# Kernel tuning notes

Measured on AMD Instinct MI355X. Metric: run time of the kernel, lower is better.

The kernel has to match this reference:

```python
import jax, jax.numpy as jnp
import numpy as np

B, S, D, H, O, E, K = 4, 2048, 1024, 2048, 1024, 8, 2

def setup_inputs() -> dict:
    key = jax.random.key(0)
    ks = jax.random.split(key, 8)
    x = jax.random.normal(ks[0], (B, S, D), dtype=jnp.float32)
    # kaiming-uniform-ish scale for weights, zero biases (as in _init_w)
    gate_w = jax.random.uniform(ks[1], (E, D), dtype=jnp.float32, minval=-1, maxval=1) * np.sqrt(6.0 / D)
    gate_b = jnp.zeros((E,), dtype=jnp.float32)
    w1 = jax.random.uniform(ks[2], (E, D, H), dtype=jnp.float32, minval=-1, maxval=1) * np.sqrt(6.0 / D)
    b1 = jnp.zeros((E, H), dtype=jnp.float32)
    w2 = jax.random.uniform(ks[3], (E, H, O), dtype=jnp.float32, minval=-1, maxval=1) * np.sqrt(6.0 / H)
    b2 = jnp.zeros((E, O), dtype=jnp.float32)
    return {"x": x, "gate_w": gate_w, "gate_b": gate_b, "w1": w1, "b1": b1, "w2": w2, "b2": b2}

def reference(x, gate_w, gate_b, w1, b1, w2, b2):
    # gate: softmax over experts, then top-k (k=2)
    logits = jnp.einsum('bsd,ed->bse', x, gate_w) + gate_b          # [B,S,E]
    probs = jax.nn.softmax(logits, axis=-1)
    topk_vals, topk_idx = jax.lax.top_k(probs, K)                    # [B,S,K]
    # dense all-expert MLPs (Linear-ReLU-Linear), dropout = 0
    h = jax.nn.relu(jnp.einsum('bsd,edh->bseh', x, w1) + b1)         # [B,S,E,H]
    expert_out = jnp.einsum('bseh,eho->bseo', h, w2) + b2            # [B,S,E,O]
    # gather top-k experts and combine with gate weights
    sel = jnp.take_along_axis(expert_out, topk_idx[..., None], axis=2)  # [B,S,K,O]
    return jnp.sum(sel * topk_vals[..., None], axis=2)               # [B,S,O]
```

## Files before the change

kernel.cpp:

```cpp
#include <hip/hip_runtime.h>

#define T_TOKENS 8192
#define D_DIM 1024
#define H_DIM 2048
#define O_DIM 1024
#define E_NUM 8
#define NPAIR 16384
#define GY_MAX 136

typedef unsigned short u16;
typedef __bf16 bf16x8 __attribute__((ext_vector_type(8)));
typedef float f32x4 __attribute__((ext_vector_type(4)));

__device__ inline u16 f2bf(float f) {
  union { float f; unsigned u; } v; v.f = f;
  unsigned r = v.u + 0x7FFFu + ((v.u >> 16) & 1u);
  return (u16)(r >> 16);
}

__device__ __forceinline__ void gload16(const u16* g, u16* l) {
  __builtin_amdgcn_global_load_lds((const __attribute__((address_space(1))) void*)g,
                                   (__attribute__((address_space(3))) void*)l, 16, 0, 0);
}

__global__ void transpose_cvt_kernel(const float* __restrict__ w, u16* __restrict__ wt,
                                     int R, int C) {
  __shared__ float tile[32][33];
  int e = blockIdx.z;
  int c0 = blockIdx.x * 32, r0 = blockIdx.y * 32;
  const float* wp = w + (size_t)e * R * C;
  u16* wtp = wt + (size_t)e * R * C;
  int tx = threadIdx.x, ty = threadIdx.y;
  #pragma unroll
  for (int j = 0; j < 32; j += 8)
    tile[ty + j][tx] = wp[(size_t)(r0 + ty + j) * C + c0 + tx];
  __syncthreads();
  #pragma unroll
  for (int j = 0; j < 32; j += 8)
    wtp[(size_t)(c0 + ty + j) * R + r0 + tx] = f2bf(tile[tx][ty + j]);
}

__global__ void gate_kernel(const float* __restrict__ x, const float* __restrict__ gw,
                            const float* __restrict__ gb, int* __restrict__ topk_idx,
                            float* __restrict__ topk_val, u16* __restrict__ xb) {
  int t = blockIdx.x * 4 + (threadIdx.x >> 6);
  int lane = threadIdx.x & 63;
  const float4* xr4 = (const float4*)(x + (size_t)t * D_DIM);
  const float4* gw4 = (const float4*)gw;
  u16* xbr = xb + (size_t)t * D_DIM;
  float acc[E_NUM];
  #pragma unroll
  for (int e = 0; e < E_NUM; e++) acc[e] = 0.f;
  #pragma unroll
  for (int it = 0; it < D_DIM / 256; ++it) {
    float4 xv = xr4[it * 64 + lane];
    ushort4 o;
    o.x = f2bf(xv.x); o.y = f2bf(xv.y); o.z = f2bf(xv.z); o.w = f2bf(xv.w);
    *(ushort4*)(xbr + (it * 64 + lane) * 4) = o;
    #pragma unroll
    for (int e = 0; e < E_NUM; e++) {
      float4 wv = gw4[e * (D_DIM / 4) + it * 64 + lane];
      acc[e] += xv.x * wv.x + xv.y * wv.y + xv.z * wv.z + xv.w * wv.w;
    }
  }
  #pragma unroll
  for (int e = 0; e < E_NUM; e++) {
    #pragma unroll
    for (int o = 32; o > 0; o >>= 1) acc[e] += __shfl_down(acc[e], o);
  }
  if (lane == 0) {
    float l[E_NUM], mx = -1e30f;
    #pragma unroll
    for (int e = 0; e < E_NUM; e++) { l[e] = acc[e] + gb[e]; mx = fmaxf(mx, l[e]); }
    float p[E_NUM], s = 0.f;
    #pragma unroll
    for (int e = 0; e < E_NUM; e++) { p[e] = expf(l[e] - mx); s += p[e]; }
    float inv = 1.f / s;
    int i1 = 0;
    #pragma unroll
    for (int e = 1; e < E_NUM; e++) if (p[e] > p[i1]) i1 = e;
    int i2 = (i1 == 0) ? 1 : 0;
    #pragma unroll
    for (int e = 0; e < E_NUM; e++) if (e != i1 && e != i2 && p[e] > p[i2]) i2 = e;
    topk_idx[t * 2] = i1;     topk_idx[t * 2 + 1] = i2;
    topk_val[t * 2] = p[i1] * inv; topk_val[t * 2 + 1] = p[i2] * inv;
  }
}

__global__ void histscan_kernel(const int* __restrict__ topk_idx,
                                int* __restrict__ counts, int* __restrict__ eoff,
                                int* __restrict__ nblk, int* __restrict__ tbl_e,
                                int* __restrict__ tbl_m0) {
  __shared__ int wh[4][E_NUM];
  int tid = threadIdx.x;
  int lane = tid & 63, wave = tid >> 6;
  int myc = 0;
  for (int i = tid; i < NPAIR; i += 256) {
    int e = topk_idx[i];
    #pragma unroll
    for (int ee = 0; ee < E_NUM; ee++) {
      unsigned long long m = __ballot(e == ee);
      if (lane == ee) myc += __popcll(m);
    }
  }
  if (lane < E_NUM) wh[wave][lane] = myc;
  __syncthreads();
  if (tid == 0) {
    int s = 0, cl[E_NUM];
    for (int e = 0; e < E_NUM; e++) {
      int c = wh[0][e] + wh[1][e] + wh[2][e] + wh[3][e];
      counts[e] = c;
      cl[e] = c;
      eoff[e] = s;
      s += c;
    }
    eoff[E_NUM] = s;
    int nb = 0;
    for (int e = 0; e < E_NUM; e++)
      for (int m0 = 0; m0 < cl[e]; m0 += 128) { tbl_e[nb] = e; tbl_m0[nb] = m0; nb++; }
    nblk[0] = nb;
  }
}

__global__ void scatter_kernel(const int* __restrict__ topk_idx, const float* __restrict__ topk_val,
                               const int* __restrict__ eoff, int* __restrict__ cursor_pad,
                               int* __restrict__ pair_token, float* __restrict__ pair_gate) {
  __shared__ int lhist[E_NUM];
  __shared__ int lbase[E_NUM];
  int tid = threadIdx.x;
  int t = blockIdx.x * 256 + tid;
  if (tid < E_NUM) lhist[tid] = 0;
  __syncthreads();
  int e0 = topk_idx[t * 2], e1 = topk_idx[t * 2 + 1];
  int r0 = atomicAdd(&lhist[e0], 1);
  int r1 = atomicAdd(&lhist[e1], 1);
  __syncthreads();
  if (tid < E_NUM) lbase[tid] = eoff[tid] + atomicAdd(&cursor_pad[tid * 32], lhist[tid]);
  __syncthreads();
  int p0 = lbase[e0] + r0;
  int p1 = lbase[e1] + r1;
  pair_token[p0] = t; pair_gate[p0] = topk_val[t * 2];
  pair_token[p1] = t; pair_gate[p1] = topk_val[t * 2 + 1];
}


__global__ __launch_bounds__(256, 2) void gemm1_kernel(
    const u16* __restrict__ xb, const u16* __restrict__ w1t, const float* __restrict__ b1,
    const int* __restrict__ pair_token, const int* __restrict__ eoff,
    const int* __restrict__ ecnt, const int* __restrict__ nblk,
    const int* __restrict__ tbl_e, const int* __restrict__ tbl_m0,
    u16* __restrict__ hbuf) {
  int lin = blockIdx.y * 16 + blockIdx.x;
  int swz = (lin & 7) * (16 * GY_MAX / 8) + (lin >> 3);
  const int bx = swz & 15;
  const int yb = swz >> 4;
  if (yb >= nblk[0]) return;
  const int e = tbl_e[yb];
  const int m0t = tbl_m0[yb];
  const int ne = ecnt[e];
  const int off = eoff[e];
  const int n0 = bx * 128;

  __shared__ __align__(16) u16 As0[128 * 64], As1[128 * 64];
  __shared__ __align__(16) u16 Bs0[128 * 64], Bs1[128 * 64];

  const int tid = threadIdx.x;
  const int wid = tid >> 6;
  const int lane = tid & 63;

  const int strow8 = lane >> 3;
  const int slot = lane & 7;
  const u16* aptr[4]; const u16* bptr[4];
  #pragma unroll
  for (int j = 0; j < 4; j++) {
    int r = wid * 32 + j * 8 + strow8;
    int gm = m0t + r;
    int tok = (gm < ne) ? pair_token[off + gm] : 0;
    int gl = slot ^ (r & 7);
    aptr[j] = xb + (size_t)tok * D_DIM + gl * 8;
    bptr[j] = w1t + ((size_t)e * H_DIM + (n0 + r)) * D_DIM + gl * 8;
  }

  const int wm = (wid & 1) * 64;
  const int wn = (wid >> 1) * 64;
  const int lrow = lane & 15;
  const int quad = lane >> 4;
  const int pg0 = quad ^ (lrow & 7);
  const int pg1 = (quad + 4) ^ (lrow & 7);

  f32x4 acc[4][4] = {};

  auto STAGE = [&](u16* A_, u16* B_, int kk) {
    #pragma unroll
    for (int j = 0; j < 4; j++) {
      gload16(aptr[j] + kk, A_ + wid * 2048 + j * 512);
      gload16(bptr[j] + kk, B_ + wid * 2048 + j * 512);
    }
  };
  auto COMPUTE = [&](const u16* A_, const u16* B_) {
    bf16x8 af[4], bfr[4];
    #pragma unroll
    for (int i = 0; i < 4; i++) af[i] = *(const bf16x8*)&A_[(wm + i * 16 + lrow) * 64 + pg0 * 8];
    #pragma unroll
    for (int j = 0; j < 4; j++) bfr[j] = *(const bf16x8*)&B_[(wn + j * 16 + lrow) * 64 + pg0 * 8];
    #pragma unroll
    for (int i = 0; i < 4; i++)
      #pragma unroll
      for (int j = 0; j < 4; j++)
        acc[i][j] = __builtin_amdgcn_mfma_f32_16x16x32_bf16(af[i], bfr[j], acc[i][j], 0, 0, 0);
    #pragma unroll
    for (int i = 0; i < 4; i++) af[i] = *(const bf16x8*)&A_[(wm + i * 16 + lrow) * 64 + pg1 * 8];
    #pragma unroll
    for (int j = 0; j < 4; j++) bfr[j] = *(const bf16x8*)&B_[(wn + j * 16 + lrow) * 64 + pg1 * 8];
    #pragma unroll
    for (int i = 0; i < 4; i++)
      #pragma unroll
      for (int j = 0; j < 4; j++)
        acc[i][j] = __builtin_amdgcn_mfma_f32_16x16x32_bf16(af[i], bfr[j], acc[i][j], 0, 0, 0);
  };

  STAGE(As0, Bs0, 0);
  __syncthreads();
  for (int k0 = 0; k0 < D_DIM; k0 += 128) {
    if (k0 + 64 < D_DIM) STAGE(As1, Bs1, k0 + 64);
    COMPUTE(As0, Bs0);
    __syncthreads();
    if (k0 + 128 < D_DIM) STAGE(As0, Bs0, k0 + 128);
    COMPUTE(As1, Bs1);
    __syncthreads();
  }

  #pragma unroll
  for (int i = 0; i < 4; i++) {
    #pragma unroll
    for (int r = 0; r < 4; r++) {
      int m = wm + i * 16 + quad * 4 + r;
      int gm = m0t + m;
      if (gm >= ne) continue;
      size_t rowbase = (size_t)(off + gm) * H_DIM;
      #pragma unroll
      for (int j = 0; j < 4; j++) {
        int n = n0 + wn + j * 16 + lrow;
        float v = acc[i][j][r] + b1[e * H_DIM + n];
        v = v > 0.f ? v : 0.f;
        hbuf[rowbase + n] = f2bf(v);
      }
    }
  }
}

__global__ __launch_bounds__(256, 2) void gemm2_kernel(
    const u16* __restrict__ hbuf, const u16* __restrict__ w2t, const float* __restrict__ b2,
    const int* __restrict__ pair_token, const float* __restrict__ pair_gate,
    const int* __restrict__ eoff, const int* __restrict__ ecnt,
    const int* __restrict__ nblk, const int* __restrict__ tbl_e,
    const int* __restrict__ tbl_m0, float* __restrict__ out) {
  int lin = blockIdx.y * 8 + blockIdx.x;
  int swz = (lin & 7) * (8 * GY_MAX / 8) + (lin >> 3);
  const int bx = swz & 7;
  const int yb = swz >> 3;
  if (yb >= nblk[0]) return;
  const int e = tbl_e[yb];
  const int m0t = tbl_m0[yb];
  const int ne = ecnt[e];
  const int off = eoff[e];
  const int n0 = bx * 128;

  __shared__ __align__(16) u16 As0[128 * 64], As1[128 * 64];
  __shared__ __align__(16) u16 Bs0[128 * 64], Bs1[128 * 64];

  const int tid = threadIdx.x;
  const int wid = tid >> 6;
  const int lane = tid & 63;

  const int strow8 = lane >> 3;
  const int slot = lane & 7;
  const u16* aptr[4]; const u16* bptr[4];
  #pragma unroll
  for (int j = 0; j < 4; j++) {
    int r = wid * 32 + j * 8 + strow8;
    int gl = slot ^ (r & 7);
    aptr[j] = hbuf + (size_t)(off + m0t + r) * H_DIM + gl * 8;
    bptr[j] = w2t + ((size_t)e * O_DIM + (n0 + r)) * H_DIM + gl * 8;
  }

  const int wm = (wid & 1) * 64;
  const int wn = (wid >> 1) * 64;
  const int lrow = lane & 15;
  const int quad = lane >> 4;
  const int pg0 = quad ^ (lrow & 7);
  const int pg1 = (quad + 4) ^ (lrow & 7);

  f32x4 acc[4][4] = {};

  auto STAGE = [&](u16* A_, u16* B_, int kk) {
    #pragma unroll
    for (int j = 0; j < 4; j++) {
      gload16(aptr[j] + kk, A_ + wid * 2048 + j * 512);
      gload16(bptr[j] + kk, B_ + wid * 2048 + j * 512);
    }
  };
  auto COMPUTE = [&](const u16* A_, const u16* B_) {
    bf16x8 af[4], bfr[4];
    #pragma unroll
    for (int i = 0; i < 4; i++) af[i] = *(const bf16x8*)&A_[(wm + i * 16 + lrow) * 64 + pg0 * 8];
    #pragma unroll
    for (int j = 0; j < 4; j++) bfr[j] = *(const bf16x8*)&B_[(wn + j * 16 + lrow) * 64 + pg0 * 8];
    #pragma unroll
    for (int i = 0; i < 4; i++)
      #pragma unroll
      for (int j = 0; j < 4; j++)
        acc[i][j] = __builtin_amdgcn_mfma_f32_16x16x32_bf16(af[i], bfr[j], acc[i][j], 0, 0, 0);
    #pragma unroll
    for (int i = 0; i < 4; i++) af[i] = *(const bf16x8*)&A_[(wm + i * 16 + lrow) * 64 + pg1 * 8];
    #pragma unroll
    for (int j = 0; j < 4; j++) bfr[j] = *(const bf16x8*)&B_[(wn + j * 16 + lrow) * 64 + pg1 * 8];
    #pragma unroll
    for (int i = 0; i < 4; i++)
      #pragma unroll
      for (int j = 0; j < 4; j++)
        acc[i][j] = __builtin_amdgcn_mfma_f32_16x16x32_bf16(af[i], bfr[j], acc[i][j], 0, 0, 0);
  };

  STAGE(As0, Bs0, 0);
  __syncthreads();
  for (int k0 = 0; k0 < H_DIM; k0 += 128) {
    if (k0 + 64 < H_DIM) STAGE(As1, Bs1, k0 + 64);
    COMPUTE(As0, Bs0);
    __syncthreads();
    if (k0 + 128 < H_DIM) STAGE(As0, Bs0, k0 + 128);
    COMPUTE(As1, Bs1);
    __syncthreads();
  }

  #pragma unroll
  for (int i = 0; i < 4; i++) {
    #pragma unroll
    for (int r = 0; r < 4; r++) {
      int m = wm + i * 16 + quad * 4 + r;
      int gm = m0t + m;
      if (gm >= ne) continue;
      int pair = off + gm;
      int tok = pair_token[pair];
      float g = pair_gate[pair];
      #pragma unroll
      for (int j = 0; j < 4; j++) {
        int n = n0 + wn + j * 16 + lrow;
        float v = (acc[i][j][r] + b2[e * O_DIM + n]) * g;
        atomicAdd(&out[(size_t)tok * O_DIM + n], v);
      }
    }
  }
}

extern "C" void kernel_launch(void* const* d_in, const int* in_sizes, int n_in,
                              void* d_out, int out_size, void* d_ws, size_t ws_size,
                              hipStream_t stream) {
  const float* x  = (const float*)d_in[0];
  const float* gw = (const float*)d_in[1];
  const float* gb = (const float*)d_in[2];
  const float* w1 = (const float*)d_in[3];
  const float* b1 = (const float*)d_in[4];
  const float* w2 = (const float*)d_in[5];
  const float* b2 = (const float*)d_in[6];
  float* out = (float*)d_out;

  char* ws = (char*)d_ws;
  size_t off = 0;
  auto take = [&](size_t bytes) -> char* {
    char* p = ws + off;
    off = (off + bytes + 255) & ~(size_t)255;
    return p;
  };
  int*   meta       = (int*)take(4096);
  int*   cursor_pad = meta;
  int*   counts     = meta + 256;
  int*   eoff       = meta + 264;
  int*   nblk       = meta + 273;
  int*   tbl_e      = meta + 274;
  int*   tbl_m0     = meta + 410;
  int*   topk_idx   = (int*)take((size_t)T_TOKENS * 2 * 4);
  float* topk_val   = (float*)take((size_t)T_TOKENS * 2 * 4);
  int*   pair_token = (int*)take((size_t)(NPAIR + 256) * 4);
  float* pair_gate  = (float*)take((size_t)(NPAIR + 256) * 4);
  u16*   xb         = (u16*)take((size_t)T_TOKENS * D_DIM * 2);
  u16*   w1t        = (u16*)take((size_t)E_NUM * D_DIM * H_DIM * 2);
  u16*   w2t        = (u16*)take((size_t)E_NUM * H_DIM * O_DIM * 2);
  u16*   hbuf       = (u16*)take((size_t)(NPAIR + 128) * H_DIM * 2);

  hipMemsetAsync(meta, 0, 4096, stream);
  hipMemsetAsync(out, 0, (size_t)T_TOKENS * O_DIM * 4, stream);

  transpose_cvt_kernel<<<dim3(H_DIM / 32, D_DIM / 32, E_NUM), dim3(32, 8), 0, stream>>>(w1, w1t, D_DIM, H_DIM);
  transpose_cvt_kernel<<<dim3(O_DIM / 32, H_DIM / 32, E_NUM), dim3(32, 8), 0, stream>>>(w2, w2t, H_DIM, O_DIM);
  gate_kernel<<<T_TOKENS / 4, 256, 0, stream>>>(x, gw, gb, topk_idx, topk_val, xb);
  histscan_kernel<<<1, 256, 0, stream>>>(topk_idx, counts, eoff, nblk, tbl_e, tbl_m0);
  scatter_kernel<<<T_TOKENS / 256, 256, 0, stream>>>(topk_idx, topk_val, eoff, cursor_pad, pair_token, pair_gate);
  gemm1_kernel<<<dim3(16, GY_MAX), 256, 0, stream>>>(xb, w1t, b1, pair_token, eoff, counts, nblk, tbl_e, tbl_m0, hbuf);
  gemm2_kernel<<<dim3(8, GY_MAX), 256, 0, stream>>>(hbuf, w2t, b2, pair_token, pair_gate, eoff, counts, nblk, tbl_e, tbl_m0, out);
}
```

Measured before the change: 523.7 us.

## Use triple-buffered K=32 LDS pipeline with vmcnt waits in expert GEMMs

Both expert GEMM kernels move from a double-buffered K=64 stage to a three-stage ring of K=32 tiles (48KB LDS total), with a new packed two-rows-per-64-element swizzled layout. Each iteration waits with explicit s_waitcnt vmcnt instead of a full drain, so two future tiles stay in flight while the current one is computed. Launch bounds rise to 3 blocks per CU to raise occupancy. The cost is twice as many barriers per K, half as many MFMAs between barriers, and reliance on hand-counted vmcnt values, which is fragile if the compiler adds or reorders memory ops.

New measurement: 498.8 us. 1.05x faster.

```diff
diff --git a/kernel.cpp b/kernel.cpp
--- a/kernel.cpp
+++ b/kernel.cpp
@@ -11,6 +11,14 @@
 typedef unsigned short u16;
 typedef __bf16 bf16x8 __attribute__((ext_vector_type(8)));
 typedef float f32x4 __attribute__((ext_vector_type(4)));
+
+#define VMCNT(n) asm volatile("s_waitcnt vmcnt(" #n ")" ::: "memory")
+
+__device__ __forceinline__ void barsync() {
+  asm volatile("" ::: "memory");
+  __builtin_amdgcn_s_barrier();
+  __builtin_amdgcn_sched_barrier(0);
+}
 
 __device__ inline u16 f2bf(float f) {
   union { float f; unsigned u; } v; v.f = f;
@@ -144,7 +152,7 @@
 }
 
 
-__global__ __launch_bounds__(256, 2) void gemm1_kernel(
+__global__ __launch_bounds__(256, 3) void gemm1_kernel(
     const u16* __restrict__ xb, const u16* __restrict__ w1t, const float* __restrict__ b1,
     const int* __restrict__ pair_token, const int* __restrict__ eoff,
     const int* __restrict__ ecnt, const int* __restrict__ nblk,
@@ -161,57 +169,59 @@
   const int off = eoff[e];
   const int n0 = bx * 128;
 
-  __shared__ __align__(16) u16 As0[128 * 64], As1[128 * 64];
-  __shared__ __align__(16) u16 Bs0[128 * 64], Bs1[128 * 64];
+  __shared__ __align__(16) u16 SH[3 * 2 * 4096];
 
   const int tid = threadIdx.x;
   const int wid = tid >> 6;
   const int lane = tid & 63;
 
-  const int strow8 = lane >> 3;
-  const int slot = lane & 7;
-  const u16* aptr[4]; const u16* bptr[4];
-  #pragma unroll
-  for (int j = 0; j < 4; j++) {
-    int r = wid * 32 + j * 8 + strow8;
+  const u16* aptrA[2]; const u16* bptrB[2];
+  #pragma unroll
+  for (int j = 0; j < 2; j++) {
+    int p = wid * 16 + j * 8 + (lane >> 3);
+    int u = (lane & 7) ^ (p & 7);
+    int r = 2 * p + (u >> 2);
+    int c = u & 3;
     int gm = m0t + r;
     int tok = (gm < ne) ? pair_token[off + gm] : 0;
-    int gl = slot ^ (r & 7);
-    aptr[j] = xb + (size_t)tok * D_DIM + gl * 8;
-    bptr[j] = w1t + ((size_t)e * H_DIM + (n0 + r)) * D_DIM + gl * 8;
+    aptrA[j] = xb + (size_t)tok * D_DIM + c * 8;
+    bptrB[j] = w1t + ((size_t)e * H_DIM + (n0 + r)) * D_DIM + c * 8;
   }
 
   const int wm = (wid & 1) * 64;
   const int wn = (wid >> 1) * 64;
   const int lrow = lane & 15;
   const int quad = lane >> 4;
-  const int pg0 = quad ^ (lrow & 7);
-  const int pg1 = (quad + 4) ^ (lrow & 7);
 
   f32x4 acc[4][4] = {};
 
-  auto STAGE = [&](u16* A_, u16* B_, int kk) {
+  auto STAGE = [&](int buf, int k0) {
+    u16* Ab = SH + buf * 8192;
+    u16* Bb = Ab + 4096;
+    #pragma unroll
+    for (int j = 0; j < 2; j++) {
+      gload16(aptrA[j] + k0, Ab + (wid * 16 + j * 8) * 64);
+      gload16(bptrB[j] + k0, Bb + (wid * 16 + j * 8) * 64);
+    }
+  };
+  auto COMPUTE = [&](int buf) {
+    const u16* Ab = SH + buf * 8192;
+    const u16* Bb = Ab + 4096;
+    bf16x8 af[4], bfr[4];
+    #pragma unroll
+    for (int i = 0; i < 4; i++) {
+      int r = wm + i * 16 + lrow;
+      int p = r >> 1;
+      int s = (((r & 1) << 2) | quad) ^ (p & 7);
+      af[i] = *(const bf16x8*)&Ab[p * 64 + s * 8];
+    }
     #pragma unroll
     for (int j = 0; j < 4; j++) {
-      gload16(aptr[j] + kk, A_ + wid * 2048 + j * 512);
-      gload16(bptr[j] + kk, B_ + wid * 2048 + j * 512);
-    }
-  };
-  auto COMPUTE = [&](const u16* A_, const u16* B_) {
-    bf16x8 af[4], bfr[4];
-    #pragma unroll
-    for (int i = 0; i < 4; i++) af[i] = *(const bf16x8*)&A_[(wm + i * 16 + lrow) * 64 + pg0 * 8];
-    #pragma unroll
-    for (int j = 0; j < 4; j++) bfr[j] = *(const bf16x8*)&B_[(wn + j * 16 + lrow) * 64 + pg0 * 8];
-    #pragma unroll
-    for (int i = 0; i < 4; i++)
-      #pragma unroll
-      for (int j = 0; j < 4; j++)
-        acc[i][j] = __builtin_amdgcn_mfma_f32_16x16x32_bf16(af[i], bfr[j], acc[i][j], 0, 0, 0);
-    #pragma unroll
-    for (int i = 0; i < 4; i++) af[i] = *(const bf16x8*)&A_[(wm + i * 16 + lrow) * 64 + pg1 * 8];
-    #pragma unroll
-    for (int j = 0; j < 4; j++) bfr[j] = *(const bf16x8*)&B_[(wn + j * 16 + lrow) * 64 + pg1 * 8];
+      int r = wn + j * 16 + lrow;
+      int p = r >> 1;
+      int s = (((r & 1) << 2) | quad) ^ (p & 7);
+      bfr[j] = *(const bf16x8*)&Bb[p * 64 + s * 8];
+    }
     #pragma unroll
     for (int i = 0; i < 4; i++)
       #pragma unroll
@@ -219,16 +229,19 @@
         acc[i][j] = __builtin_amdgcn_mfma_f32_16x16x32_bf16(af[i], bfr[j], acc[i][j], 0, 0, 0);
   };
 
-  STAGE(As0, Bs0, 0);
-  __syncthreads();
-  for (int k0 = 0; k0 < D_DIM; k0 += 128) {
-    if (k0 + 64 < D_DIM) STAGE(As1, Bs1, k0 + 64);
-    COMPUTE(As0, Bs0);
-    __syncthreads();
-    if (k0 + 128 < D_DIM) STAGE(As0, Bs0, k0 + 128);
-    COMPUTE(As1, Bs1);
-    __syncthreads();
-  }
+  STAGE(0, 0); STAGE(1, 32); STAGE(2, 64);
+  int cur = 0;
+  for (int t = 0; t < D_DIM / 32 - 3; ++t) {
+    VMCNT(8);
+    barsync();
+    COMPUTE(cur);
+    barsync();
+    STAGE(cur, (t + 3) * 32);
+    cur = (cur == 2) ? 0 : cur + 1;
+  }
+  VMCNT(8); barsync(); COMPUTE(cur); cur = (cur == 2) ? 0 : cur + 1;
+  VMCNT(4); barsync(); COMPUTE(cur); cur = (cur == 2) ? 0 : cur + 1;
+  VMCNT(0); barsync(); COMPUTE(cur);
 
   #pragma unroll
   for (int i = 0; i < 4; i++) {
@@ -249,7 +262,7 @@
   }
 }
 
-__global__ __launch_bounds__(256, 2) void gemm2_kernel(
+__global__ __launch_bounds__(256, 3) void gemm2_kernel(
     const u16* __restrict__ hbuf, const u16* __restrict__ w2t, const float* __restrict__ b2,
     const int* __restrict__ pair_token, const float* __restrict__ pair_gate,
     const int* __restrict__ eoff, const int* __restrict__ ecnt,
@@ -266,55 +279,57 @@
   const int off = eoff[e];
   const int n0 = bx * 128;
 
-  __shared__ __align__(16) u16 As0[128 * 64], As1[128 * 64];
-  __shared__ __align__(16) u16 Bs0[128 * 64], Bs1[128 * 64];
+  __shared__ __align__(16) u16 SH[3 * 2 * 4096];
 
   const int tid = threadIdx.x;
   const int wid = tid >> 6;
   const int lane = tid & 63;
 
-  const int strow8 = lane >> 3;
-  const int slot = lane & 7;
-  const u16* aptr[4]; const u16* bptr[4];
-  #pragma unroll
-  for (int j = 0; j < 4; j++) {
-    int r = wid * 32 + j * 8 + strow8;
-    int gl = slot ^ (r & 7);
-    aptr[j] = hbuf + (size_t)(off + m0t + r) * H_DIM + gl * 8;
-    bptr[j] = w2t + ((size_t)e * O_DIM + (n0 + r)) * H_DIM + gl * 8;
+  const u16* aptrA[2]; const u16* bptrB[2];
+  #pragma unroll
+  for (int j = 0; j < 2; j++) {
+    int p = wid * 16 + j * 8 + (lane >> 3);
+    int u = (lane & 7) ^ (p & 7);
+    int r = 2 * p + (u >> 2);
+    int c = u & 3;
+    aptrA[j] = hbuf + (size_t)(off + m0t + r) * H_DIM + c * 8;
+    bptrB[j] = w2t + ((size_t)e * O_DIM + (n0 + r)) * H_DIM + c * 8;
   }
 
   const int wm = (wid & 1) * 64;
   const int wn = (wid >> 1) * 64;
   const int lrow = lane & 15;
   const int quad = lane >> 4;
-  const int pg0 = quad ^ (lrow & 7);
-  const int pg1 = (quad + 4) ^ (lrow & 7);
 
   f32x4 acc[4][4] = {};
 
-  auto STAGE = [&](u16* A_, u16* B_, int kk) {
+  auto STAGE = [&](int buf, int k0) {
+    u16* Ab = SH + buf * 8192;
+    u16* Bb = Ab + 4096;
+    #pragma unroll
+    for (int j = 0; j < 2; j++) {
+      gload16(aptrA[j] + k0, Ab + (wid * 16 + j * 8) * 64);
+      gload16(bptrB[j] + k0, Bb + (wid * 16 + j * 8) * 64);
+    }
+  };
+  auto COMPUTE = [&](int buf) {
+    const u16* Ab = SH + buf * 8192;
+    const u16* Bb = Ab + 4096;
+    bf16x8 af[4], bfr[4];
+    #pragma unroll
+    for (int i = 0; i < 4; i++) {
+      int r = wm + i * 16 + lrow;
+      int p = r >> 1;
+      int s = (((r & 1) << 2) | quad) ^ (p & 7);
+      af[i] = *(const bf16x8*)&Ab[p * 64 + s * 8];
+    }
     #pragma unroll
     for (int j = 0; j < 4; j++) {
-      gload16(aptr[j] + kk, A_ + wid * 2048 + j * 512);
-      gload16(bptr[j] + kk, B_ + wid * 2048 + j * 512);
-    }
-  };
-  auto COMPUTE = [&](const u16* A_, const u16* B_) {
-    bf16x8 af[4], bfr[4];
-    #pragma unroll
-    for (int i = 0; i < 4; i++) af[i] = *(const bf16x8*)&A_[(wm + i * 16 + lrow) * 64 + pg0 * 8];
-    #pragma unroll
-    for (int j = 0; j < 4; j++) bfr[j] = *(const bf16x8*)&B_[(wn + j * 16 + lrow) * 64 + pg0 * 8];
-    #pragma unroll
-    for (int i = 0; i < 4; i++)
-      #pragma unroll
-      for (int j = 0; j < 4; j++)
-        acc[i][j] = __builtin_amdgcn_mfma_f32_16x16x32_bf16(af[i], bfr[j], acc[i][j], 0, 0, 0);
-    #pragma unroll
-    for (int i = 0; i < 4; i++) af[i] = *(const bf16x8*)&A_[(wm + i * 16 + lrow) * 64 + pg1 * 8];
-    #pragma unroll
-    for (int j = 0; j < 4; j++) bfr[j] = *(const bf16x8*)&B_[(wn + j * 16 + lrow) * 64 + pg1 * 8];
+      int r = wn + j * 16 + lrow;
+      int p = r >> 1;
+      int s = (((r & 1) << 2) | quad) ^ (p & 7);
+      bfr[j] = *(const bf16x8*)&Bb[p * 64 + s * 8];
+    }
     #pragma unroll
     for (int i = 0; i < 4; i++)
       #pragma unroll
@@ -322,16 +337,19 @@
         acc[i][j] = __builtin_amdgcn_mfma_f32_16x16x32_bf16(af[i], bfr[j], acc[i][j], 0, 0, 0);
   };
 
-  STAGE(As0, Bs0, 0);
-  __syncthreads();
-  for (int k0 = 0; k0 < H_DIM; k0 += 128) {
-    if (k0 + 64 < H_DIM) STAGE(As1, Bs1, k0 + 64);
-    COMPUTE(As0, Bs0);
-    __syncthreads();
-    if (k0 + 128 < H_DIM) STAGE(As0, Bs0, k0 + 128);
-    COMPUTE(As1, Bs1);
-    __syncthreads();
-  }
+  STAGE(0, 0); STAGE(1, 32); STAGE(2, 64);
+  int cur = 0;
+  for (int t = 0; t < H_DIM / 32 - 3; ++t) {
+    VMCNT(8);
+    barsync();
+    COMPUTE(cur);
+    barsync();
+    STAGE(cur, (t + 3) * 32);
+    cur = (cur == 2) ? 0 : cur + 1;
+  }
+  VMCNT(8); barsync(); COMPUTE(cur); cur = (cur == 2) ? 0 : cur + 1;
+  VMCNT(4); barsync(); COMPUTE(cur); cur = (cur == 2) ? 0 : cur + 1;
+  VMCNT(0); barsync(); COMPUTE(cur);
 
   #pragma unroll
   for (int i = 0; i < 4; i++) {
```
